# Kernel tuning notes

Hardware: AMD Instinct MI355X
Metric: run time of the kernel (lower is better)

Reference implementation:

```python
import jax, jax.numpy as jnp
import numpy as np

B, N, D_IN, H, L, HEADS = 8, 1024, 64, 128, 2, 4
HEAD_DIM = H // HEADS
EPS = 1e-5


def setup_inputs() -> dict:
    key = jax.random.key(0)
    ks = jax.random.split(key, 20)
    x = jax.random.normal(ks[0], (B, N, D_IN), dtype=jnp.float32)
    adj = jax.random.randint(ks[1], (B, N, N), 0, 2).astype(jnp.float32)
    s = lambda fan_in: 1.0 / np.sqrt(fan_in)
    enc_w = jax.random.uniform(ks[2], (H, D_IN), minval=-s(D_IN), maxval=s(D_IN))
    enc_b = jax.random.uniform(ks[3], (H,), minval=-s(D_IN), maxval=s(D_IN))
    # per-layer stacked projection weights, torch Linear layout [out,in]
    def mk(k, shape):
        return jax.random.uniform(k, shape, minval=-s(H), maxval=s(H))
    q_w = mk(ks[4], (L, H, H)); q_b = mk(ks[5], (L, H))
    k_w = mk(ks[6], (L, H, H)); k_b = mk(ks[7], (L, H))
    v_w = mk(ks[8], (L, H, H)); v_b = mk(ks[9], (L, H))
    o_w = mk(ks[10], (L, H, H)); o_b = mk(ks[11], (L, H))
    ln_g = jnp.ones((L, H), jnp.float32)
    ln_b = jnp.zeros((L, H), jnp.float32)
    out_w = mk(ks[12], (H, H)); out_b = mk(ks[13], (H,))
    return {"x": x, "adj": adj, "enc_w": enc_w, "enc_b": enc_b,
            "q_w": q_w, "q_b": q_b, "k_w": k_w, "k_b": k_b,
            "v_w": v_w, "v_b": v_b, "o_w": o_w, "o_b": o_b,
            "ln_g": ln_g, "ln_b": ln_b, "out_w": out_w, "out_b": out_b}


def _layernorm(x, g, b):
    mu = jnp.mean(x, axis=-1, keepdims=True)
    var = jnp.var(x, axis=-1, keepdims=True)
    return (x - mu) * jax.lax.rsqrt(var + EPS) * g + b


def _gat_layer(h, adj, qw, qb, kw, kb, vw, vb, ow, ob):
    b, n, _ = h.shape
    q = (h @ qw.T + qb).reshape(b, n, HEADS, HEAD_DIM)
    k = (h @ kw.T + kb).reshape(b, n, HEADS, HEAD_DIM)
    v = (h @ vw.T + vb).reshape(b, n, HEADS, HEAD_DIM)
    scale = HEAD_DIM ** -0.5
    attn = jnp.einsum('bihd,bjhd->bhij', q, k) * scale
    mask = adj[:, None, :, :]  # (b,1,n,n)
    attn = jnp.where(mask == 0, -jnp.inf, attn)
    a = jax.nn.softmax(attn, axis=-1)
    a = jnp.nan_to_num(a, nan=0.0)  # rows with no neighbours -> 0
    out = jnp.einsum('bhij,bjhd->bihd', a, v).reshape(b, n, H)
    return out @ ow.T + ob


def reference(x, adj, enc_w, enc_b, q_w, q_b, k_w, k_b, v_w, v_b,
              o_w, o_b, ln_g, ln_b, out_w, out_b):
    h = jax.nn.relu(x @ enc_w.T + enc_b)
    for i in range(L):
        h_new = _gat_layer(h, adj, q_w[i], q_b[i], k_w[i], k_b[i],
                           v_w[i], v_b[i], o_w[i], o_b[i])
        h = jax.nn.relu(_layernorm(h_new, ln_g[i], ln_b[i])) + h
    return h @ out_w.T + out_b
```

## Files before the change

kernel.cpp:

```cpp
#include <hip/hip_runtime.h>

#define B 8
#define N 1024
#define D_IN 64
#define H 128
#define HEADS 4
#define HD 32
#define L 2
#define EPS 1e-5f
#define NEG_BIG -1e30f
#define QSCALE (0.17677669529663687f * 1.4426950408889634f)

typedef __attribute__((ext_vector_type(8))) short bf16x8;
typedef __attribute__((ext_vector_type(4))) float f32x4;

__device__ __forceinline__ unsigned short f2bf(float f) {
    unsigned u = __float_as_uint(f);
    u = u + 0x7fffu + ((u >> 16) & 1u);
    return (unsigned short)(u >> 16);
}
__device__ __forceinline__ float bf2f(unsigned short s) {
    return __uint_as_float(((unsigned)s) << 16);
}
__device__ __forceinline__ void gload_lds16(const void* g, void* l) {
    __builtin_amdgcn_global_load_lds(
        (const __attribute__((address_space(1))) unsigned int*)g,
        (__attribute__((address_space(3))) unsigned int*)l,
        16, 0, 0);
}

__global__ __launch_bounds__(256) void pack_kernel(
    const float* __restrict__ adj, unsigned* __restrict__ mb) {
    int wd = blockIdx.x * 256 + threadIdx.x;
    const float4* src = (const float4*)(adj + (size_t)wd * 32);
    unsigned m = 0;
    #pragma unroll
    for (int c = 0; c < 8; ++c) {
        float4 f = src[c];
        if (f.x != 0.0f) m |= 1u << (c * 4 + 0);
        if (f.y != 0.0f) m |= 1u << (c * 4 + 1);
        if (f.z != 0.0f) m |= 1u << (c * 4 + 2);
        if (f.w != 0.0f) m |= 1u << (c * 4 + 3);
    }
    mb[wd] = m;
}

__global__ __launch_bounds__(256) void prep_kernel(
    const float* __restrict__ x, const float* __restrict__ enc_w,
    const float* __restrict__ q_w, const float* __restrict__ k_w,
    const float* __restrict__ v_w, const float* __restrict__ q_b,
    const float* __restrict__ k_b, const float* __restrict__ v_b,
    const float* __restrict__ o_w, const float* __restrict__ out_w,
    unsigned short* __restrict__ x_bf, unsigned short* __restrict__ wenc,
    unsigned short* __restrict__ wqkv, float* __restrict__ bqkv,
    unsigned short* __restrict__ woh, unsigned short* __restrict__ wol,
    unsigned short* __restrict__ wfh, unsigned short* __restrict__ wfl) {
    int id = blockIdx.x * 256 + threadIdx.x;
    const int XN = B * N * D_IN;
    const int WE = H * D_IN;
    const int WQ = L * 3 * H * H;
    const int BQ = L * 3 * H;
    const int WO = L * H * H;
    const int WF = H * H;
    if (id < XN) { x_bf[id] = f2bf(x[id]); return; }
    id -= XN;
    if (id < WE) { wenc[id] = f2bf(enc_w[id]); return; }
    id -= WE;
    if (id < WQ) {
        int layer = id / (3 * H * H);
        int r = id % (3 * H * H);
        int mat = r / (H * H);
        int e = r % (H * H);
        const float* src = mat == 0 ? q_w : (mat == 1 ? k_w : v_w);
        float f = src[layer * H * H + e];
        if (mat == 0) f *= QSCALE;
        wqkv[id] = f2bf(f);
        return;
    }
    id -= WQ;
    if (id < BQ) {
        int layer = id / (3 * H);
        int r = id % (3 * H);
        int mat = r / H;
        int e = r % H;
        const float* src = mat == 0 ? q_b : (mat == 1 ? k_b : v_b);
        float f = src[layer * H + e];
        if (mat == 0) f *= QSCALE;
        bqkv[id] = f;
        return;
    }
    id -= BQ;
    if (id < WO) {
        float f = o_w[id];
        unsigned short hi = f2bf(f);
        woh[id] = hi;
        wol[id] = f2bf(f - bf2f(hi));
        return;
    }
    id -= WO;
    if (id < WF) {
        float f = out_w[id];
        unsigned short hi = f2bf(f);
        wfh[id] = hi;
        wfl[id] = f2bf(f - bf2f(hi));
    }
}

__global__ __launch_bounds__(256) void enc_kernel(
    const unsigned short* __restrict__ x_bf, const unsigned short* __restrict__ wenc,
    const float* __restrict__ eb, float* __restrict__ h, unsigned short* __restrict__ h_bf) {
    __shared__ unsigned short wt[H * D_IN];
    __shared__ unsigned short at[32 * D_IN];
    const int t = threadIdx.x;
    const int r0 = blockIdx.x * 32;
    const int w = t >> 6, lane = t & 63, g = lane >> 4, c16 = lane & 15;
    const int rw = w & 1, chw = w >> 1;

    #pragma unroll
    for (int i = 0; i < 4; ++i) {
        int ci = i * 256 + t, row = ci >> 3, cr = ci & 7;
        gload_lds16(wenc + row * 64 + (cr ^ (row & 7)) * 8, (char*)wt + (i * 4 + w) * 1024);
    }
    {
        int row = t >> 3, cr = t & 7;
        gload_lds16(x_bf + (size_t)(r0 + row) * 64 + (cr ^ (row & 7)) * 8,
                    (char*)at + w * 1024);
    }
    __syncthreads();

    const int arow = rw * 16 + c16;
    bf16x8 a0 = *(const bf16x8*)(at + arow * 64 + ((g ^ (arow & 7)) * 8));
    bf16x8 a1 = *(const bf16x8*)(at + arow * 64 + (((4 + g) ^ (arow & 7)) * 8));
    f32x4 acc[4];
    #pragma unroll
    for (int sub = 0; sub < 4; ++sub) {
        int bcol = chw * 64 + sub * 16 + c16;
        bf16x8 b0 = *(const bf16x8*)(wt + bcol * 64 + ((g ^ (bcol & 7)) * 8));
        bf16x8 b1 = *(const bf16x8*)(wt + bcol * 64 + (((4 + g) ^ (bcol & 7)) * 8));
        f32x4 z = {0.f, 0.f, 0.f, 0.f};
        z = __builtin_amdgcn_mfma_f32_16x16x32_bf16(a0, b0, z, 0, 0, 0);
        acc[sub] = __builtin_amdgcn_mfma_f32_16x16x32_bf16(a1, b1, z, 0, 0, 0);
    }
    #pragma unroll
    for (int sub = 0; sub < 4; ++sub) {
        int col = chw * 64 + sub * 16 + c16;
        float bias = eb[col];
        #pragma unroll
        for (int rr = 0; rr < 4; ++rr) {
            int row = r0 + rw * 16 + g * 4 + rr;
            float v = fmaxf(acc[sub][rr] + bias, 0.0f);
            h[(size_t)row * H + col] = v;
            h_bf[(size_t)row * H + col] = f2bf(v);
        }
    }
}

__global__ __launch_bounds__(256) void qkv_kernel(
    const unsigned short* __restrict__ h_bf, const unsigned short* __restrict__ wqkv_l,
    const float* __restrict__ bqkv_l,
    unsigned short* __restrict__ q, unsigned short* __restrict__ k,
    unsigned short* __restrict__ vT) {
    __shared__ unsigned short wt[192 * 128];
    __shared__ unsigned short at[64 * 128];
    const int t = threadIdx.x;
    const int r0 = (blockIdx.x >> 1) * 64;
    const int ch = blockIdx.x & 1;
    const int w = t >> 6, lane = t & 63, g = lane >> 4, c16 = lane & 15;
    const unsigned short* wsrc = wqkv_l + (size_t)ch * 192 * 128;

    #pragma unroll
    for (int i = 0; i < 12; ++i) {
        int ci = i * 256 + t, row = ci >> 4, cr = ci & 15;
        gload_lds16(wsrc + (size_t)row * 128 + (cr ^ (row & 7)) * 8,
                    (char*)wt + (i * 4 + w) * 1024);
    }
    #pragma unroll
    for (int i = 0; i < 4; ++i) {
        int ci = i * 256 + t, row = ci >> 4, cr = ci & 15;
        gload_lds16(h_bf + (size_t)(r0 + row) * 128 + (cr ^ (row & 7)) * 8,
                    (char*)at + (i * 4 + w) * 1024);
    }
    __syncthreads();

    const int arow = w * 16 + c16;
    bf16x8 a[4];
    #pragma unroll
    for (int ks = 0; ks < 4; ++ks)
        a[ks] = *(const bf16x8*)(at + arow * 128 + (((ks * 4 + g) ^ (arow & 7)) * 8));

    f32x4 acc[12];
    #pragma unroll
    for (int sub = 0; sub < 12; ++sub) {
        int bcol = sub * 16 + c16;
        f32x4 z = {0.f, 0.f, 0.f, 0.f};
        #pragma unroll
        for (int ks = 0; ks < 4; ++ks) {
            bf16x8 bb = *(const bf16x8*)(wt + (size_t)bcol * 128 + (((ks * 4 + g) ^ (bcol & 7)) * 8));
            z = __builtin_amdgcn_mfma_f32_16x16x32_bf16(a[ks], bb, z, 0, 0, 0);
        }
        acc[sub] = z;
    }
    #pragma unroll
    for (int sub = 0; sub < 12; ++sub) {
        int gcol = ch * 192 + sub * 16 + c16;
        int mat = gcol >> 7;
        int colin = gcol & 127;
        float bias = bqkv_l[mat * H + colin];
        if (mat < 2) {
            unsigned short* dst = mat == 0 ? q : k;
            #pragma unroll
            for (int rr = 0; rr < 4; ++rr) {
                int row = r0 + w * 16 + g * 4 + rr;
                dst[(size_t)row * H + colin] = f2bf(acc[sub][rr] + bias);
            }
        } else {
            int hd = colin >> 5, d = colin & 31;
            int bb = r0 >> 10;
            int jbase = (r0 & (N - 1)) + w * 16 + g * 4;
            int pos = (jbase & ~63) + ((((jbase >> 3) & 7) ^ (d & 7)) << 3) + (jbase & 7);
            float v0 = acc[sub][0] + bias, v1 = acc[sub][1] + bias;
            float v2 = acc[sub][2] + bias, v3 = acc[sub][3] + bias;
            unsigned lo, hi;
            asm("v_cvt_pk_bf16_f32 %0, %1, %2" : "=v"(lo) : "v"(v0), "v"(v1));
            asm("v_cvt_pk_bf16_f32 %0, %1, %2" : "=v"(hi) : "v"(v2), "v"(v3));
            uint2 pk2; pk2.x = lo; pk2.y = hi;
            *(uint2*)(vT + ((size_t)(bb * HEADS + hd) * HD + d) * N + pos) = pk2;
        }
    }
}

__global__ __launch_bounds__(256) void attn_kernel(
    const unsigned short* __restrict__ qg, const unsigned short* __restrict__ kg,
    const unsigned short* __restrict__ vTg, const unsigned* __restrict__ mb,
    float* __restrict__ ao) {
    __shared__ unsigned short qt[64 * 32];
    __shared__ unsigned short kt[2][128 * 32];
    __shared__ unsigned short vt[2][32 * 128];
    __shared__ unsigned short pl[4][16 * 136];

    const int bid = blockIdx.x;
    const int itile = bid & 15;
    const int head = (bid >> 4) & 3;
    const int b = bid >> 6;
    const int i0 = itile * 64;
    const int bh = b * HEADS + head;

    const int t = threadIdx.x;
    const int w = t >> 6;
    const int lane = t & 63;
    const int g = lane >> 4;
    const int c16 = lane & 15;

    const int srow = t >> 2;
    const int sch = (t & 3) ^ ((t >> 2) & 3);

    gload_lds16(qg + ((size_t)(b * N + i0 + srow)) * H + head * HD + sch * 8,
                (char*)qt + w * 1024);
    #pragma unroll
    for (int i = 0; i < 2; ++i)
        gload_lds16(kg + ((size_t)(b * N + i * 64 + srow)) * H + head * HD + sch * 8,
                    (char*)kt[0] + i * 4096 + w * 1024);
    #pragma unroll
    for (int i = 0; i < 2; ++i) {
        int d = i * 16 + (t >> 4), c = t & 15;
        gload_lds16(vTg + ((size_t)bh * HD + d) * N + c * 8,
                    (char*)vt[0] + i * 4096 + w * 1024);
    }
    const unsigned* mrow = mb + (size_t)(b * N + i0 + w * 16 + c16) * (N / 32);
    uint4 am = *(const uint4*)mrow;

    __syncthreads();

    const int swq = c16 & 3;
    const bf16x8 qfrag = *(const bf16x8*)(qt + (w * 16 + c16) * 32 + ((g ^ swq) * 8));

    f32x4 oacc[2];
    oacc[0] = (f32x4){0.f, 0.f, 0.f, 0.f};
    oacc[1] = (f32x4){0.f, 0.f, 0.f, 0.f};
    float mrun = NEG_BIG, lrun = 0.0f;

    for (int jt = 0; jt < 8; ++jt) {
        const int cur = jt & 1;
        uint4 amn;
        if (jt < 7) {
            const int j0n = (jt + 1) * 128;
            #pragma unroll
            for (int i = 0; i < 2; ++i)
                gload_lds16(kg + ((size_t)(b * N + j0n + i * 64 + srow)) * H + head * HD + sch * 8,
                            (char*)kt[cur ^ 1] + i * 4096 + w * 1024);
            #pragma unroll
            for (int i = 0; i < 2; ++i) {
                int d = i * 16 + (t >> 4), c = t & 15;
                gload_lds16(vTg + ((size_t)bh * HD + d) * N + j0n + c * 8,
                            (char*)vt[cur ^ 1] + i * 4096 + w * 1024);
            }
            amn = *(const uint4*)(mrow + (jt + 1) * 4);
        }
        f32x4 sacc[8];
        __builtin_amdgcn_s_setprio(1);
        #pragma unroll
        for (int jsub = 0; jsub < 8; ++jsub) {
            bf16x8 kfrag = *(const bf16x8*)(kt[cur] + (jsub * 16 + c16) * 32 + ((g ^ swq) * 8));
            f32x4 z = {0.f, 0.f, 0.f, 0.f};
            sacc[jsub] = __builtin_amdgcn_mfma_f32_16x16x32_bf16(kfrag, qfrag, z, 0, 0, 0);
        }
        __builtin_amdgcn_s_setprio(0);
        float mx = NEG_BIG;
        #pragma unroll
        for (int jsub = 0; jsub < 8; ++jsub) {
            int wsel = jsub >> 1;
            unsigned mw = wsel == 0 ? am.x : wsel == 1 ? am.y : wsel == 2 ? am.z : am.w;
            #pragma unroll
            for (int r = 0; r < 4; ++r) {
                bool alive = (mw >> ((jsub & 1) * 16 + g * 4 + r)) & 1u;
                float s = alive ? sacc[jsub][r] : NEG_BIG;
                sacc[jsub][r] = s;
                mx = fmaxf(mx, s);
            }
        }
        mx = fmaxf(mx, __shfl_xor(mx, 16));
        mx = fmaxf(mx, __shfl_xor(mx, 32));
        float mnew = fmaxf(mrun, mx);
        float sf = exp2f(mrun - mnew);
        mrun = mnew;
        float rs = 0.0f;
        #pragma unroll
        for (int jsub = 0; jsub < 8; ++jsub)
            #pragma unroll
            for (int r = 0; r < 4; ++r) {
                float pv = exp2f(sacc[jsub][r] - mnew);
                sacc[jsub][r] = pv;
                rs += pv;
            }
        rs += __shfl_xor(rs, 16);
        rs += __shfl_xor(rs, 32);
        lrun = lrun * sf + rs;
        #pragma unroll
        for (int jsub = 0; jsub < 8; ++jsub) {
            unsigned lo, hi;
            asm("v_cvt_pk_bf16_f32 %0, %1, %2" : "=v"(lo) : "v"(sacc[jsub][0]), "v"(sacc[jsub][1]));
            asm("v_cvt_pk_bf16_f32 %0, %1, %2" : "=v"(hi) : "v"(sacc[jsub][2]), "v"(sacc[jsub][3]));
            uint2 pk2; pk2.x = lo; pk2.y = hi;
            *(uint2*)(&pl[w][c16 * 136 + jsub * 16 + g * 4]) = pk2;
        }
        #pragma unroll
        for (int dsub = 0; dsub < 2; ++dsub)
            #pragma unroll
            for (int r = 0; r < 4; ++r)
                oacc[dsub][r] *= sf;
        asm volatile("s_waitcnt lgkmcnt(0)" ::: "memory");
        __builtin_amdgcn_s_setprio(1);
        #pragma unroll
        for (int ks = 0; ks < 4; ++ks) {
            bf16x8 pa = *(const bf16x8*)(&pl[w][c16 * 136 + ks * 32 + g * 8]);
            #pragma unroll
            for (int dsub = 0; dsub < 2; ++dsub) {
                int cj = ks * 4 + g;
                bf16x8 va = *(const bf16x8*)(vt[cur] + (dsub * 16 + c16) * 128 +
                                             (cj >> 3) * 64 + (((cj & 7) ^ (c16 & 7)) * 8));
                oacc[dsub] = __builtin_amdgcn_mfma_f32_16x16x32_bf16(va, pa, oacc[dsub], 0, 0, 0);
            }
        }
        __builtin_amdgcn_s_setprio(0);
        if (jt < 7) {
            am = amn;
            __syncthreads();
        }
    }
    float inv = (lrun > 0.0f) ? (1.0f / lrun) : 0.0f;
    #pragma unroll
    for (int dsub = 0; dsub < 2; ++dsub) {
        float4 o;
        o.x = oacc[dsub][0] * inv; o.y = oacc[dsub][1] * inv;
        o.z = oacc[dsub][2] * inv; o.w = oacc[dsub][3] * inv;
        *(float4*)(ao + ((size_t)(b * N + i0 + w * 16 + c16)) * H +
                   head * HD + dsub * 16 + g * 4) = o;
    }
}

__device__ __forceinline__ void stage_split32(
    const float* __restrict__ src, unsigned short* hi, unsigned short* lo, int t) {
    #pragma unroll
    for (int it = 0; it < 4; ++it) {
        int idx4 = it * 256 + t;
        int row = idx4 >> 5, c4 = (idx4 & 31) * 4;
        float4 f = ((const float4*)src)[idx4];
        unsigned short h0 = f2bf(f.x), h1 = f2bf(f.y), h2 = f2bf(f.z), h3 = f2bf(f.w);
        unsigned short l0 = f2bf(f.x - bf2f(h0)), l1 = f2bf(f.y - bf2f(h1));
        unsigned short l2 = f2bf(f.z - bf2f(h2)), l3 = f2bf(f.w - bf2f(h3));
        *(unsigned*)(hi + row * 130 + c4)     = (unsigned)h0 | ((unsigned)h1 << 16);
        *(unsigned*)(hi + row * 130 + c4 + 2) = (unsigned)h2 | ((unsigned)h3 << 16);
        *(unsigned*)(lo + row * 130 + c4)     = (unsigned)l0 | ((unsigned)l1 << 16);
        *(unsigned*)(lo + row * 130 + c4 + 2) = (unsigned)l2 | ((unsigned)l3 << 16);
    }
}

__device__ __forceinline__ void split_gemm4(
    const unsigned short* ah, const unsigned short* al,
    const unsigned short* wh, const unsigned short* wl,
    int arow, int g, int c16, int bcol0, f32x4* acc) {
    bf16x8 ahf[4], alf[4];
    #pragma unroll
    for (int ks = 0; ks < 4; ++ks) {
        ahf[ks] = *(const bf16x8*)(ah + arow * 130 + ks * 32 + g * 8);
        alf[ks] = *(const bf16x8*)(al + arow * 130 + ks * 32 + g * 8);
    }
    #pragma unroll
    for (int sub = 0; sub < 4; ++sub) {
        int bcol = bcol0 + sub * 16 + c16;
        f32x4 z = {0.f, 0.f, 0.f, 0.f};
        #pragma unroll
        for (int ks = 0; ks < 4; ++ks) {
            bf16x8 bh = *(const bf16x8*)(wh + bcol * 128 + (((ks * 4 + g) ^ (bcol & 7)) * 8));
            bf16x8 bl = *(const bf16x8*)(wl + bcol * 128 + (((ks * 4 + g) ^ (bcol & 7)) * 8));
            z = __builtin_amdgcn_mfma_f32_16x16x32_bf16(ahf[ks], bh, z, 0, 0, 0);
            z = __builtin_amdgcn_mfma_f32_16x16x32_bf16(alf[ks], bh, z, 0, 0, 0);
            z = __builtin_amdgcn_mfma_f32_16x16x32_bf16(ahf[ks], bl, z, 0, 0, 0);
        }
        acc[sub] = z;
    }
}

__device__ __forceinline__ void stage_w(const unsigned short* __restrict__ src,
                                        unsigned short* dst, int t, int w) {
    #pragma unroll
    for (int i = 0; i < 8; ++i) {
        int ci = i * 256 + t, row = ci >> 4, cr = ci & 15;
        gload_lds16(src + (size_t)row * 128 + (cr ^ (row & 7)) * 8,
                    (char*)dst + (i * 4 + w) * 1024);
    }
}

__global__ __launch_bounds__(256) void oln_kernel(
    const float* __restrict__ ao, const unsigned short* __restrict__ woh_l,
    const unsigned short* __restrict__ wol_l, const float* __restrict__ ob,
    const float* __restrict__ lng, const float* __restrict__ lnb,
    float* __restrict__ h, unsigned short* __restrict__ h_bf) {
    __shared__ unsigned short ah[32 * 130], al[32 * 130];
    __shared__ unsigned short wh[128 * 128], wl[128 * 128];
    __shared__ float red1[2][32], red2[2][32];
    const int t = threadIdx.x;
    const int r0 = blockIdx.x * 32;
    const int w = t >> 6, lane = t & 63, g = lane >> 4, c16 = lane & 15;
    const int rw = w & 1, chw = w >> 1;

    stage_w(woh_l, wh, t, w);
    stage_w(wol_l, wl, t, w);
    stage_split32(ao + (size_t)r0 * H, ah, al, t);
    __syncthreads();

    const int arow = rw * 16 + c16;
    f32x4 acc[4];
    split_gemm4(ah, al, wh, wl, arow, g, c16, chw * 64, acc);

    float val[4][4], s1[4] = {0, 0, 0, 0}, s2[4] = {0, 0, 0, 0};
    #pragma unroll
    for (int sub = 0; sub < 4; ++sub) {
        int col = chw * 64 + sub * 16 + c16;
        float bias = ob[col];
        #pragma unroll
        for (int rr = 0; rr < 4; ++rr) {
            float vv = acc[sub][rr] + bias;
            val[sub][rr] = vv;
            s1[rr] += vv;
            s2[rr] += vv * vv;
        }
    }
    #pragma unroll
    for (int rr = 0; rr < 4; ++rr) {
        #pragma unroll
        for (int off = 1; off < 16; off <<= 1) {
            s1[rr] += __shfl_xor(s1[rr], off);
            s2[rr] += __shfl_xor(s2[rr], off);
        }
    }
    if (c16 == 0) {
        #pragma unroll
        for (int rr = 0; rr < 4; ++rr) {
            red1[chw][rw * 16 + g * 4 + rr] = s1[rr];
            red2[chw][rw * 16 + g * 4 + rr] = s2[rr];
        }
    }
    __syncthreads();
    #pragma unroll
    for (int rr = 0; rr < 4; ++rr) {
        int rl = rw * 16 + g * 4 + rr;
        float t1 = red1[0][rl] + red1[1][rl];
        float t2 = red2[0][rl] + red2[1][rl];
        float mu = t1 * (1.0f / H);
        float var = t2 * (1.0f / H) - mu * mu;
        float rsn = rsqrtf(var + EPS);
        int row = r0 + rl;
        #pragma unroll
        for (int sub = 0; sub < 4; ++sub) {
            int col = chw * 64 + sub * 16 + c16;
            float y = (val[sub][rr] - mu) * rsn * lng[col] + lnb[col];
            float hn = fmaxf(y, 0.0f) + h[(size_t)row * H + col];
            h[(size_t)row * H + col] = hn;
            h_bf[(size_t)row * H + col] = f2bf(hn);
        }
    }
}

__global__ __launch_bounds__(256) void olnfinal_kernel(
    const float* __restrict__ ao, const unsigned short* __restrict__ woh_l,
    const unsigned short* __restrict__ wol_l, const float* __restrict__ ob,
    const float* __restrict__ lng, const float* __restrict__ lnb,
    const float* __restrict__ h, const unsigned short* __restrict__ wfh,
    const unsigned short* __restrict__ wfl, const float* __restrict__ fb,
    float* __restrict__ out) {
    __shared__ unsigned short ah[32 * 130], al[32 * 130];
    __shared__ unsigned short wh[128 * 128], wl[128 * 128];
    __shared__ float red1[2][32], red2[2][32];
    const int t = threadIdx.x;
    const int r0 = blockIdx.x * 32;
    const int w = t >> 6, lane = t & 63, g = lane >> 4, c16 = lane & 15;
    const int rw = w & 1, chw = w >> 1;

    stage_w(woh_l, wh, t, w);
    stage_w(wol_l, wl, t, w);
    stage_split32(ao + (size_t)r0 * H, ah, al, t);
    __syncthreads();

    const int arow = rw * 16 + c16;
    f32x4 acc[4];
    split_gemm4(ah, al, wh, wl, arow, g, c16, chw * 64, acc);

    float val[4][4], s1[4] = {0, 0, 0, 0}, s2[4] = {0, 0, 0, 0};
    #pragma unroll
    for (int sub = 0; sub < 4; ++sub) {
        int col = chw * 64 + sub * 16 + c16;
        float bias = ob[col];
        #pragma unroll
        for (int rr = 0; rr < 4; ++rr) {
            float vv = acc[sub][rr] + bias;
            val[sub][rr] = vv;
            s1[rr] += vv;
            s2[rr] += vv * vv;
        }
    }
    #pragma unroll
    for (int rr = 0; rr < 4; ++rr) {
        #pragma unroll
        for (int off = 1; off < 16; off <<= 1) {
            s1[rr] += __shfl_xor(s1[rr], off);
            s2[rr] += __shfl_xor(s2[rr], off);
        }
    }
    if (c16 == 0) {
        #pragma unroll
        for (int rr = 0; rr < 4; ++rr) {
            red1[chw][rw * 16 + g * 4 + rr] = s1[rr];
            red2[chw][rw * 16 + g * 4 + rr] = s2[rr];
        }
    }
    __syncthreads();
    #pragma unroll
    for (int rr = 0; rr < 4; ++rr) {
        int rl = rw * 16 + g * 4 + rr;
        float t1 = red1[0][rl] + red1[1][rl];
        float t2 = red2[0][rl] + red2[1][rl];
        float mu = t1 * (1.0f / H);
        float var = t2 * (1.0f / H) - mu * mu;
        float rsn = rsqrtf(var + EPS);
        #pragma unroll
        for (int sub = 0; sub < 4; ++sub) {
            int col = chw * 64 + sub * 16 + c16;
            float y = (val[sub][rr] - mu) * rsn * lng[col] + lnb[col];
            float hn = fmaxf(y, 0.0f) + h[(size_t)(r0 + rl) * H + col];
            unsigned short hi = f2bf(hn);
            ah[rl * 130 + col] = hi;
            al[rl * 130 + col] = f2bf(hn - bf2f(hi));
        }
    }
    stage_w(wfh, wh, t, w);
    stage_w(wfl, wl, t, w);
    __syncthreads();

    f32x4 fac[4];
    split_gemm4(ah, al, wh, wl, arow, g, c16, chw * 64, fac);
    #pragma unroll
    for (int sub = 0; sub < 4; ++sub) {
        int col = chw * 64 + sub * 16 + c16;
        float bias = fb[col];
        #pragma unroll
        for (int rr = 0; rr < 4; ++rr) {
            int row = r0 + rw * 16 + g * 4 + rr;
            out[(size_t)row * H + col] = fac[sub][rr] + bias;
        }
    }
}

extern "C" void kernel_launch(void* const* d_in, const int* in_sizes, int n_in,
                              void* d_out, int out_size, void* d_ws, size_t ws_size,
                              hipStream_t stream) {
    const float* x     = (const float*)d_in[0];
    const float* adj   = (const float*)d_in[1];
    const float* enc_w = (const float*)d_in[2];
    const float* enc_b = (const float*)d_in[3];
    const float* q_w   = (const float*)d_in[4];
    const float* q_b   = (const float*)d_in[5];
    const float* k_w   = (const float*)d_in[6];
    const float* k_b   = (const float*)d_in[7];
    const float* v_w   = (const float*)d_in[8];
    const float* v_b   = (const float*)d_in[9];
    const float* o_w   = (const float*)d_in[10];
    const float* o_b   = (const float*)d_in[11];
    const float* ln_g  = (const float*)d_in[12];
    const float* ln_b  = (const float*)d_in[13];
    const float* out_w = (const float*)d_in[14];
    const float* out_b = (const float*)d_in[15];

    const size_t BNH = (size_t)B * N * H;
    float* h  = (float*)d_ws;
    float* ao = h + BNH;
    unsigned short* h_bf = (unsigned short*)(ao + BNH);
    unsigned short* qb = h_bf + BNH;
    unsigned short* kb = qb + BNH;
    unsigned short* vT = kb + BNH;
    unsigned* mbits = (unsigned*)(vT + BNH);
    unsigned short* x_bf = (unsigned short*)(mbits + (size_t)B * N * N / 32);
    unsigned short* wenc = x_bf + (size_t)B * N * D_IN;
    unsigned short* wqkv = wenc + H * D_IN;
    float* bqkv = (float*)(wqkv + (size_t)L * 3 * H * H);
    unsigned short* woh = (unsigned short*)(bqkv + L * 3 * H);
    unsigned short* wol = woh + (size_t)L * H * H;
    unsigned short* wfh = wol + (size_t)L * H * H;
    unsigned short* wfl = wfh + (size_t)H * H;

    pack_kernel<<<B * N * N / 32 / 256, 256, 0, stream>>>(adj, mbits);
    const int prep_total = B * N * D_IN + H * D_IN + L * 3 * H * H + L * 3 * H
                         + L * H * H + H * H;
    prep_kernel<<<(prep_total + 255) / 256, 256, 0, stream>>>(
        x, enc_w, q_w, k_w, v_w, q_b, k_b, v_b, o_w, out_w,
        x_bf, wenc, wqkv, bqkv, woh, wol, wfh, wfl);
    enc_kernel<<<B * N / 32, 256, 0, stream>>>(x_bf, wenc, enc_b, h, h_bf);

    qkv_kernel<<<B * N / 32, 256, 0, stream>>>(h_bf, wqkv, bqkv, qb, kb, vT);
    attn_kernel<<<B * HEADS * (N / 64), 256, 0, stream>>>(qb, kb, vT, mbits, ao);
    oln_kernel<<<B * N / 32, 256, 0, stream>>>(
        ao, woh, wol, o_b, ln_g, ln_b, h, h_bf);
    qkv_kernel<<<B * N / 32, 256, 0, stream>>>(
        h_bf, wqkv + (size_t)3 * H * H, bqkv + 3 * H, qb, kb, vT);
    attn_kernel<<<B * HEADS * (N / 64), 256, 0, stream>>>(qb, kb, vT, mbits, ao);
    olnfinal_kernel<<<B * N / 32, 256, 0, stream>>>(
        ao, woh + (size_t)H * H, wol + (size_t)H * H, o_b + H,
        ln_g + H, ln_b + H, h, wfh, wfl, out_b, (float*)d_out);
}
```

Measured before the change: 95.43 us.

## Merge pack, prep and encoder into one launch and shrink attention tiles

The adjacency bit-packing, weight conversion and encoder GEMM now run in one front kernel whose blocks are partitioned by blockIdx. The encoder converts fp32 x and enc_w to bf16 directly into LDS, which removes the x_bf/wenc intermediates and two launches. The attention kernel moves to 128-thread blocks covering 32 query rows with 64-key tiles, doubling the grid and halving LDS per block. The cost is more loop iterations and more reloads of K/V across blocks. Placing the encoder blocks inside the same grid also relies on prep finishing before later kernels, which stream ordering guarantees.

Result: slower. 99.82 us (+4.6%).

```diff
diff --git a/kernel.cpp b/kernel.cpp
--- a/kernel.cpp
+++ b/kernel.cpp
@@ -29,102 +29,108 @@
         16, 0, 0);
 }
 
-__global__ __launch_bounds__(256) void pack_kernel(
-    const float* __restrict__ adj, unsigned* __restrict__ mb) {
-    int wd = blockIdx.x * 256 + threadIdx.x;
-    const float4* src = (const float4*)(adj + (size_t)wd * 32);
-    unsigned m = 0;
-    #pragma unroll
-    for (int c = 0; c < 8; ++c) {
-        float4 f = src[c];
-        if (f.x != 0.0f) m |= 1u << (c * 4 + 0);
-        if (f.y != 0.0f) m |= 1u << (c * 4 + 1);
-        if (f.z != 0.0f) m |= 1u << (c * 4 + 2);
-        if (f.w != 0.0f) m |= 1u << (c * 4 + 3);
-    }
-    mb[wd] = m;
-}
-
-__global__ __launch_bounds__(256) void prep_kernel(
-    const float* __restrict__ x, const float* __restrict__ enc_w,
+#define NPACK 1024
+#define NPREP 579
+#define NENC  256
+
+__global__ __launch_bounds__(256) void front_kernel(
+    const float* __restrict__ adj, const float* __restrict__ x,
+    const float* __restrict__ enc_w, const float* __restrict__ eb,
     const float* __restrict__ q_w, const float* __restrict__ k_w,
     const float* __restrict__ v_w, const float* __restrict__ q_b,
     const float* __restrict__ k_b, const float* __restrict__ v_b,
     const float* __restrict__ o_w, const float* __restrict__ out_w,
-    unsigned short* __restrict__ x_bf, unsigned short* __restrict__ wenc,
-    unsigned short* __restrict__ wqkv, float* __restrict__ bqkv,
-    unsigned short* __restrict__ woh, unsigned short* __restrict__ wol,
-    unsigned short* __restrict__ wfh, unsigned short* __restrict__ wfl) {
-    int id = blockIdx.x * 256 + threadIdx.x;
-    const int XN = B * N * D_IN;
-    const int WE = H * D_IN;
-    const int WQ = L * 3 * H * H;
-    const int BQ = L * 3 * H;
-    const int WO = L * H * H;
-    const int WF = H * H;
-    if (id < XN) { x_bf[id] = f2bf(x[id]); return; }
-    id -= XN;
-    if (id < WE) { wenc[id] = f2bf(enc_w[id]); return; }
-    id -= WE;
-    if (id < WQ) {
-        int layer = id / (3 * H * H);
-        int r = id % (3 * H * H);
-        int mat = r / (H * H);
-        int e = r % (H * H);
-        const float* src = mat == 0 ? q_w : (mat == 1 ? k_w : v_w);
-        float f = src[layer * H * H + e];
-        if (mat == 0) f *= QSCALE;
-        wqkv[id] = f2bf(f);
-        return;
-    }
-    id -= WQ;
-    if (id < BQ) {
-        int layer = id / (3 * H);
-        int r = id % (3 * H);
-        int mat = r / H;
-        int e = r % H;
-        const float* src = mat == 0 ? q_b : (mat == 1 ? k_b : v_b);
-        float f = src[layer * H + e];
-        if (mat == 0) f *= QSCALE;
-        bqkv[id] = f;
-        return;
-    }
-    id -= BQ;
-    if (id < WO) {
-        float f = o_w[id];
-        unsigned short hi = f2bf(f);
-        woh[id] = hi;
-        wol[id] = f2bf(f - bf2f(hi));
-        return;
-    }
-    id -= WO;
-    if (id < WF) {
-        float f = out_w[id];
-        unsigned short hi = f2bf(f);
-        wfh[id] = hi;
-        wfl[id] = f2bf(f - bf2f(hi));
-    }
-}
-
-__global__ __launch_bounds__(256) void enc_kernel(
-    const unsigned short* __restrict__ x_bf, const unsigned short* __restrict__ wenc,
-    const float* __restrict__ eb, float* __restrict__ h, unsigned short* __restrict__ h_bf) {
+    unsigned* __restrict__ mb, unsigned short* __restrict__ wqkv,
+    float* __restrict__ bqkv, unsigned short* __restrict__ woh,
+    unsigned short* __restrict__ wol, unsigned short* __restrict__ wfh,
+    unsigned short* __restrict__ wfl, float* __restrict__ h,
+    unsigned short* __restrict__ h_bf) {
     __shared__ unsigned short wt[H * D_IN];
     __shared__ unsigned short at[32 * D_IN];
+    const int blk = blockIdx.x;
     const int t = threadIdx.x;
-    const int r0 = blockIdx.x * 32;
+
+    if (blk < NPACK) {
+        int wd = blk * 256 + t;
+        const float4* src = (const float4*)(adj + (size_t)wd * 32);
+        unsigned m = 0;
+        #pragma unroll
+        for (int c = 0; c < 8; ++c) {
+            float4 f = src[c];
+            if (f.x != 0.0f) m |= 1u << (c * 4 + 0);
+            if (f.y != 0.0f) m |= 1u << (c * 4 + 1);
+            if (f.z != 0.0f) m |= 1u << (c * 4 + 2);
+            if (f.w != 0.0f) m |= 1u << (c * 4 + 3);
+        }
+        mb[wd] = m;
+        return;
+    }
+    if (blk < NPACK + NPREP) {
+        int id = (blk - NPACK) * 256 + t;
+        const int WQ = L * 3 * H * H;
+        const int BQ = L * 3 * H;
+        const int WO = L * H * H;
+        if (id < WQ) {
+            int layer = id / (3 * H * H);
+            int r = id % (3 * H * H);
+            int mat = r / (H * H);
+            int e = r % (H * H);
+            const float* src = mat == 0 ? q_w : (mat == 1 ? k_w : v_w);
+            float f = src[layer * H * H + e];
+            if (mat == 0) f *= QSCALE;
+            wqkv[id] = f2bf(f);
+            return;
+        }
+        id -= WQ;
+        if (id < BQ) {
+            int layer = id / (3 * H);
+            int r = id % (3 * H);
+            int mat = r / H;
+            int e = r % H;
+            const float* src = mat == 0 ? q_b : (mat == 1 ? k_b : v_b);
+            float f = src[layer * H + e];
+            if (mat == 0) f *= QSCALE;
+            bqkv[id] = f;
+            return;
+        }
+        id -= BQ;
+        if (id < WO) {
+            float f = o_w[id];
+            unsigned short hi = f2bf(f);
+            woh[id] = hi;
+            wol[id] = f2bf(f - bf2f(hi));
+            return;
+        }
+        id -= WO;
+        {
+            float f = out_w[id];
+            unsigned short hi = f2bf(f);
+            wfh[id] = hi;
+            wfl[id] = f2bf(f - bf2f(hi));
+        }
+        return;
+    }
+    const int r0 = (blk - NPACK - NPREP) * 32;
     const int w = t >> 6, lane = t & 63, g = lane >> 4, c16 = lane & 15;
     const int rw = w & 1, chw = w >> 1;
 
     #pragma unroll
-    for (int i = 0; i < 4; ++i) {
-        int ci = i * 256 + t, row = ci >> 3, cr = ci & 7;
-        gload_lds16(wenc + row * 64 + (cr ^ (row & 7)) * 8, (char*)wt + (i * 4 + w) * 1024);
-    }
-    {
-        int row = t >> 3, cr = t & 7;
-        gload_lds16(x_bf + (size_t)(r0 + row) * 64 + (cr ^ (row & 7)) * 8,
-                    (char*)at + w * 1024);
+    for (int i = 0; i < 8; ++i) {
+        int idx4 = i * 256 + t;
+        int row = idx4 >> 4, c4 = (idx4 & 15) * 4;
+        float4 f = ((const float4*)enc_w)[idx4];
+        int off = row * 64 + (((c4 >> 3) ^ (row & 7)) * 8) + (c4 & 7);
+        wt[off] = f2bf(f.x); wt[off + 1] = f2bf(f.y);
+        wt[off + 2] = f2bf(f.z); wt[off + 3] = f2bf(f.w);
+    }
+    #pragma unroll
+    for (int i = 0; i < 2; ++i) {
+        int idx4 = i * 256 + t;
+        int row = idx4 >> 4, c4 = (idx4 & 15) * 4;
+        float4 f = ((const float4*)(x + (size_t)r0 * D_IN))[idx4];
+        int off = row * 64 + (((c4 >> 3) ^ (row & 7)) * 8) + (c4 & 7);
+        at[off] = f2bf(f.x); at[off + 1] = f2bf(f.y);
+        at[off + 2] = f2bf(f.z); at[off + 3] = f2bf(f.w);
     }
     __syncthreads();
 
@@ -229,20 +235,20 @@
     }
 }
 
-__global__ __launch_bounds__(256) void attn_kernel(
+__global__ __launch_bounds__(128) void attn_kernel(
     const unsigned short* __restrict__ qg, const unsigned short* __restrict__ kg,
     const unsigned short* __restrict__ vTg, const unsigned* __restrict__ mb,
     float* __restrict__ ao) {
-    __shared__ unsigned short qt[64 * 32];
-    __shared__ unsigned short kt[2][128 * 32];
-    __shared__ unsigned short vt[2][32 * 128];
-    __shared__ unsigned short pl[4][16 * 136];
+    __shared__ unsigned short qt[32 * 32];
+    __shared__ unsigned short kt[2][64 * 32];
+    __shared__ unsigned short vt[2][32 * 64];
+    __shared__ unsigned short pl[2][16 * 72];
 
     const int bid = blockIdx.x;
-    const int itile = bid & 15;
-    const int head = (bid >> 4) & 3;
-    const int b = bid >> 6;
-    const int i0 = itile * 64;
+    const int itile = bid & 31;
+    const int head = (bid >> 5) & 3;
+    const int b = bid >> 7;
+    const int i0 = itile * 32;
     const int bh = b * HEADS + head;
 
     const int t = threadIdx.x;
@@ -258,16 +264,15 @@
                 (char*)qt + w * 1024);
     #pragma unroll
     for (int i = 0; i < 2; ++i)
-        gload_lds16(kg + ((size_t)(b * N + i * 64 + srow)) * H + head * HD + sch * 8,
-                    (char*)kt[0] + i * 4096 + w * 1024);
-    #pragma unroll
-    for (int i = 0; i < 2; ++i) {
-        int d = i * 16 + (t >> 4), c = t & 15;
-        gload_lds16(vTg + ((size_t)bh * HD + d) * N + c * 8,
-                    (char*)vt[0] + i * 4096 + w * 1024);
-    }
+        gload_lds16(kg + ((size_t)(b * N + i * 32 + srow)) * H + head * HD + sch * 8,
+                    (char*)kt[0] + i * 2048 + w * 1024);
+    #pragma unroll
+    for (int i = 0; i < 2; ++i)
+        gload_lds16(vTg + ((size_t)bh * HD + i * 16 + (t >> 3)) * N + (t & 7) * 8,
+                    (char*)vt[0] + i * 2048 + w * 1024);
+
     const unsigned* mrow = mb + (size_t)(b * N + i0 + w * 16 + c16) * (N / 32);
-    uint4 am = *(const uint4*)mrow;
+    unsigned long long am = *(const unsigned long long*)mrow;
 
     __syncthreads();
 
@@ -279,45 +284,41 @@
     oacc[1] = (f32x4){0.f, 0.f, 0.f, 0.f};
     float mrun = NEG_BIG, lrun = 0.0f;
 
-    for (int jt = 0; jt < 8; ++jt) {
+    for (int jt = 0; jt < 16; ++jt) {
         const int cur = jt & 1;
-        uint4 amn;
-        if (jt < 7) {
-            const int j0n = (jt + 1) * 128;
+        unsigned long long amn;
+        if (jt < 15) {
+            const int j0n = (jt + 1) * 64;
             #pragma unroll
             for (int i = 0; i < 2; ++i)
-                gload_lds16(kg + ((size_t)(b * N + j0n + i * 64 + srow)) * H + head * HD + sch * 8,
-                            (char*)kt[cur ^ 1] + i * 4096 + w * 1024);
+                gload_lds16(kg + ((size_t)(b * N + j0n + i * 32 + srow)) * H + head * HD + sch * 8,
+                            (char*)kt[cur ^ 1] + i * 2048 + w * 1024);
             #pragma unroll
-            for (int i = 0; i < 2; ++i) {
-                int d = i * 16 + (t >> 4), c = t & 15;
-                gload_lds16(vTg + ((size_t)bh * HD + d) * N + j0n + c * 8,
-                            (char*)vt[cur ^ 1] + i * 4096 + w * 1024);
-            }
-            amn = *(const uint4*)(mrow + (jt + 1) * 4);
-        }
-        f32x4 sacc[8];
+            for (int i = 0; i < 2; ++i)
+                gload_lds16(vTg + ((size_t)bh * HD + i * 16 + (t >> 3)) * N + j0n + (t & 7) * 8,
+                            (char*)vt[cur ^ 1] + i * 2048 + w * 1024);
+            amn = *(const unsigned long long*)(mrow + (jt + 1) * 2);
+        }
+        f32x4 sacc[4];
         __builtin_amdgcn_s_setprio(1);
         #pragma unroll
-        for (int jsub = 0; jsub < 8; ++jsub) {
+        for (int jsub = 0; jsub < 4; ++jsub) {
             bf16x8 kfrag = *(const bf16x8*)(kt[cur] + (jsub * 16 + c16) * 32 + ((g ^ swq) * 8));
             f32x4 z = {0.f, 0.f, 0.f, 0.f};
             sacc[jsub] = __builtin_amdgcn_mfma_f32_16x16x32_bf16(kfrag, qfrag, z, 0, 0, 0);
         }
         __builtin_amdgcn_s_setprio(0);
+        unsigned long long amg = am >> (g * 4);
         float mx = NEG_BIG;
         #pragma unroll
-        for (int jsub = 0; jsub < 8; ++jsub) {
-            int wsel = jsub >> 1;
-            unsigned mw = wsel == 0 ? am.x : wsel == 1 ? am.y : wsel == 2 ? am.z : am.w;
+        for (int jsub = 0; jsub < 4; ++jsub)
             #pragma unroll
             for (int r = 0; r < 4; ++r) {
-                bool alive = (mw >> ((jsub & 1) * 16 + g * 4 + r)) & 1u;
+                bool alive = (amg >> (jsub * 16 + r)) & 1ull;
                 float s = alive ? sacc[jsub][r] : NEG_BIG;
                 sacc[jsub][r] = s;
                 mx = fmaxf(mx, s);
             }
-        }
         mx = fmaxf(mx, __shfl_xor(mx, 16));
         mx = fmaxf(mx, __shfl_xor(mx, 32));
         float mnew = fmaxf(mrun, mx);
@@ -325,7 +326,7 @@
         mrun = mnew;
         float rs = 0.0f;
         #pragma unroll
-        for (int jsub = 0; jsub < 8; ++jsub)
+        for (int jsub = 0; jsub < 4; ++jsub)
             #pragma unroll
             for (int r = 0; r < 4; ++r) {
                 float pv = exp2f(sacc[jsub][r] - mnew);
@@ -336,12 +337,12 @@
         rs += __shfl_xor(rs, 32);
         lrun = lrun * sf + rs;
         #pragma unroll
-        for (int jsub = 0; jsub < 8; ++jsub) {
+        for (int jsub = 0; jsub < 4; ++jsub) {
             unsigned lo, hi;
             asm("v_cvt_pk_bf16_f32 %0, %1, %2" : "=v"(lo) : "v"(sacc[jsub][0]), "v"(sacc[jsub][1]));
             asm("v_cvt_pk_bf16_f32 %0, %1, %2" : "=v"(hi) : "v"(sacc[jsub][2]), "v"(sacc[jsub][3]));
             uint2 pk2; pk2.x = lo; pk2.y = hi;
-            *(uint2*)(&pl[w][c16 * 136 + jsub * 16 + g * 4]) = pk2;
+            *(uint2*)(&pl[w][c16 * 72 + jsub * 16 + g * 4]) = pk2;
         }
         #pragma unroll
         for (int dsub = 0; dsub < 2; ++dsub)
@@ -351,18 +352,17 @@
         asm volatile("s_waitcnt lgkmcnt(0)" ::: "memory");
         __builtin_amdgcn_s_setprio(1);
         #pragma unroll
-        for (int ks = 0; ks < 4; ++ks) {
-            bf16x8 pa = *(const bf16x8*)(&pl[w][c16 * 136 + ks * 32 + g * 8]);
+        for (int ks = 0; ks < 2; ++ks) {
+            bf16x8 pa = *(const bf16x8*)(&pl[w][c16 * 72 + ks * 32 + g * 8]);
             #pragma unroll
             for (int dsub = 0; dsub < 2; ++dsub) {
-                int cj = ks * 4 + g;
-                bf16x8 va = *(const bf16x8*)(vt[cur] + (dsub * 16 + c16) * 128 +
-                                             (cj >> 3) * 64 + (((cj & 7) ^ (c16 & 7)) * 8));
+                bf16x8 va = *(const bf16x8*)(vt[cur] + (dsub * 16 + c16) * 64 +
+                                             (((ks * 4 + g) ^ (c16 & 7)) * 8));
                 oacc[dsub] = __builtin_amdgcn_mfma_f32_16x16x32_bf16(va, pa, oacc[dsub], 0, 0, 0);
             }
         }
         __builtin_amdgcn_s_setprio(0);
-        if (jt < 7) {
+        if (jt < 15) {
             am = amn;
             __syncthreads();
         }
@@ -619,30 +619,24 @@
     unsigned short* kb = qb + BNH;
     unsigned short* vT = kb + BNH;
     unsigned* mbits = (unsigned*)(vT + BNH);
-    unsigned short* x_bf = (unsigned short*)(mbits + (size_t)B * N * N / 32);
-    unsigned short* wenc = x_bf + (size_t)B * N * D_IN;
-    unsigned short* wqkv = wenc + H * D_IN;
+    unsigned short* wqkv = (unsigned short*)(mbits + (size_t)B * N * N / 32);
     float* bqkv = (float*)(wqkv + (size_t)L * 3 * H * H);
     unsigned short* woh = (unsigned short*)(bqkv + L * 3 * H);
     unsigned short* wol = woh + (size_t)L * H * H;
     unsigned short* wfh = wol + (size_t)L * H * H;
     unsigned short* wfl = wfh + (size_t)H * H;
 
-    pack_kernel<<<B * N * N / 32 / 256, 256, 0, stream>>>(adj, mbits);
-    const int prep_total = B * N * D_IN + H * D_IN + L * 3 * H * H + L * 3 * H
-                         + L * H * H + H * H;
-    prep_kernel<<<(prep_total + 255) / 256, 256, 0, stream>>>(
-        x, enc_w, q_w, k_w, v_w, q_b, k_b, v_b, o_w, out_w,
-        x_bf, wenc, wqkv, bqkv, woh, wol, wfh, wfl);
-    enc_kernel<<<B * N / 32, 256, 0, stream>>>(x_bf, wenc, enc_b, h, h_bf);
+    front_kernel<<<NPACK + NPREP + NENC, 256, 0, stream>>>(
+        adj, x, enc_w, enc_b, q_w, k_w, v_w, q_b, k_b, v_b, o_w, out_w,
+        mbits, wqkv, bqkv, woh, wol, wfh, wfl, h, h_bf);
 
     qkv_kernel<<<B * N / 32, 256, 0, stream>>>(h_bf, wqkv, bqkv, qb, kb, vT);
-    attn_kernel<<<B * HEADS * (N / 64), 256, 0, stream>>>(qb, kb, vT, mbits, ao);
+    attn_kernel<<<B * HEADS * (N / 32), 128, 0, stream>>>(qb, kb, vT, mbits, ao);
     oln_kernel<<<B * N / 32, 256, 0, stream>>>(
         ao, woh, wol, o_b, ln_g, ln_b, h, h_bf);
     qkv_kernel<<<B * N / 32, 256, 0, stream>>>(
         h_bf, wqkv + (size_t)3 * H * H, bqkv + 3 * H, qb, kb, vT);
-    attn_kernel<<<B * HEADS * (N / 64), 256, 0, stream>>>(qb, kb, vT, mbits, ao);
+    attn_kernel<<<B * HEADS * (N / 32), 128, 0, stream>>>(qb, kb, vT, mbits, ao);
     olnfinal_kernel<<<B * N / 32, 256, 0, stream>>>(
         ao, woh + (size_t)H * H, wol + (size_t)H * H, o_b + H,
         ln_g + H, ln_b + H, h, wfh, wfl, out_b, (float*)d_out);
```
